# Performance work log

Measured on AMD Instinct MI355X. Metric: run time of the kernel, lower is better.

Reference implementation:

```python
import jax, jax.numpy as jnp
import numpy as np

KERNEL_MUL = 2.0
KERNEL_NUM = 5


def setup_inputs() -> dict:
    key = jax.random.key(0)
    k1, k2 = jax.random.split(key)
    N, D = 4096, 256
    source = jax.random.normal(k1, (N, D), dtype=jnp.float32)
    target = jax.random.normal(k2, (N, D), dtype=jnp.float32)
    return {"source": source, "target": target}


def _gaussian_kernel_sum(source, target):
    # total: [2N, D]
    total = jnp.concatenate([source, target], axis=0)
    n = total.shape[0]
    sq = jnp.sum(total * total, axis=1)  # [2N]
    L2 = sq[:, None] + sq[None, :] - 2.0 * (total @ total.T)  # [2N, 2N]
    # Bandwidth from detached mean of off-diagonal-normalized sum (torch uses .data)
    bandwidth = jax.lax.stop_gradient(jnp.sum(L2)) / (n * n - n)
    bandwidth = bandwidth / (KERNEL_MUL ** (KERNEL_NUM // 2))
    kernels = sum(
        jnp.exp(-L2 / (bandwidth * (KERNEL_MUL ** i))) for i in range(KERNEL_NUM)
    )
    return kernels


def reference(source, target):
    b = source.shape[0]
    K = _gaussian_kernel_sum(source, target)
    XX = jnp.mean(K[:b, :b])
    YY = jnp.mean(K[b:, b:])
    XY = jnp.mean(K[:b, b:])
    YX = jnp.mean(K[b:, :b])
    return XX + YY - XY - YX
```

## Files before the change

### kernel.cpp

```cpp
#include <hip/hip_runtime.h>


#define NROWS 8192
#define HALF  4096
#define DIM   256
#define CONVB 256
#define NTILE 1056

typedef __bf16 bf16x8 __attribute__((ext_vector_type(8)));
typedef float f32x4 __attribute__((ext_vector_type(4)));
typedef unsigned short ushort8 __attribute__((ext_vector_type(8)));

__device__ __forceinline__ const float* row_ptr(const float* src, const float* tgt, int r) {
    return (r < HALF) ? (src + (size_t)r * DIM) : (tgt + (size_t)(r - HALF) * DIM);
}

__device__ __forceinline__ unsigned short bf16_rne(float x) {
    unsigned int u = __builtin_bit_cast(unsigned int, x);
    return (unsigned short)((u + 0x7FFFu + ((u >> 16) & 1u)) >> 16);
}

__global__ __launch_bounds__(256) void k_conv(const float* __restrict__ src,
                                              const float* __restrict__ tgt,
                                              unsigned short* __restrict__ hi,
                                              float* __restrict__ sq,
                                              float* __restrict__ part,
                                              double* __restrict__ parts1,
                                              float* __restrict__ out) {
    __shared__ __align__(16) unsigned short sh_hi[32 * 32 * 8];
    __shared__ float4 cs[4][64];
    __shared__ double s1s[4];

    int w = threadIdx.x >> 6, lane = threadIdx.x & 63;
    int r0 = blockIdx.x * 32;
    int g  = lane >> 1, j = lane & 1;

    float4 v[8];
    #pragma unroll
    for (int i = 0; i < 8; ++i) {
        int row = r0 + w * 8 + i;
        v[i] = ((const float4*)row_ptr(src, tgt, row))[lane];
    }

    float4 csum = {0.f, 0.f, 0.f, 0.f};
    double s1w = 0.0;
    #pragma unroll
    for (int i = 0; i < 8; ++i) {
        int rl  = w * 8 + i;
        float xs[4] = {v[i].x, v[i].y, v[i].z, v[i].w};
        unsigned short hs[4];
        #pragma unroll
        for (int k = 0; k < 4; ++k) hs[k] = bf16_rne(xs[k]);
        ushort4 h4 = {hs[0], hs[1], hs[2], hs[3]};
        int so = (g * 32 + rl) * 8 + j * 4;
        *(ushort4*)&sh_hi[so] = h4;
        csum.x += xs[0]; csum.y += xs[1]; csum.z += xs[2]; csum.w += xs[3];
        float s = xs[0] * xs[0] + xs[1] * xs[1] + xs[2] * xs[2] + xs[3] * xs[3];
        #pragma unroll
        for (int off = 32; off; off >>= 1) s += __shfl_xor(s, off, 64);
        if (lane == 0) { sq[r0 + rl] = s; s1w += (double)s; }
    }
    __syncthreads();
    int panel = blockIdx.x >> 2, quarter = blockIdx.x & 3;
    #pragma unroll
    for (int c = threadIdx.x; c < 1024; c += 256) {
        int gg = c >> 5, r = c & 31;
        size_t goff = (((size_t)panel * 32 + gg) * 128 + quarter * 32 + r) * 8;
        *(ushort8*)&hi[goff] = *(const ushort8*)&sh_hi[c * 8];
    }
    cs[w][lane] = csum;
    if (lane == 0) s1s[w] = s1w;
    __syncthreads();
    if (w == 0) {
        float4 a = cs[0][lane], b = cs[1][lane], c = cs[2][lane], d = cs[3][lane];
        float4 tot = {a.x + b.x + c.x + d.x, a.y + b.y + c.y + d.y,
                      a.z + b.z + c.z + d.z, a.w + b.w + c.w + d.w};
        *(float4*)&part[(size_t)blockIdx.x * DIM + lane * 4] = tot;
        if (lane == 0) parts1[blockIdx.x] = s1s[0] + s1s[1] + s1s[2] + s1s[3];
    }
    if (blockIdx.x == 0 && threadIdx.x == 0) out[0] = 0.0f;
}

__global__ __launch_bounds__(256) void k_scale(const double* __restrict__ parts1,
                                               const float* __restrict__ part,
                                               float* __restrict__ scale) {
    __shared__ double sh[256];
    int t = threadIdx.x;
    sh[t] = parts1[t];
    __syncthreads();
    for (int off = 128; off; off >>= 1) {
        if (t < off) sh[t] += sh[t + off];
        __syncthreads();
    }
    double S1 = sh[0];
    __syncthreads();
    float c0 = 0.f, c1 = 0.f, c2 = 0.f, c3 = 0.f;
    #pragma unroll 16
    for (int b = 0; b < CONVB; b += 4) {
        c0 += part[(b + 0) * DIM + t];
        c1 += part[(b + 1) * DIM + t];
        c2 += part[(b + 2) * DIM + t];
        c3 += part[(b + 3) * DIM + t];
    }
    double c = (double)((c0 + c1) + (c2 + c3));
    sh[t] = c * c;
    __syncthreads();
    for (int off = 128; off; off >>= 1) {
        if (t < off) sh[t] += sh[t + off];
        __syncthreads();
    }
    if (t == 0) {
        double S2    = sh[0];
        double n     = (double)NROWS;
        double sumL2 = 2.0 * n * S1 - 2.0 * S2;
        double bw    = sumL2 / (n * n - n) / 4.0;
        *scale = (float)(-1.0 / (16.0 * bw * 0.69314718055994530942));
    }
}

__global__ __launch_bounds__(256, 2) void k_pairs(const unsigned short* __restrict__ hi,
                                                  const float* __restrict__ sq,
                                                  const float* __restrict__ scale_p,
                                                  float* __restrict__ out) {
    int id = blockIdx.x;
    int I = 0;
    for (;;) {
        int cnt = 64 - 2 * I;
        if (id < cnt) break;
        id -= cnt; ++I;
    }
    int J = 2 * I + id;

    __shared__ float wsum[4];

    int t    = threadIdx.x;
    int lane = t & 63;
    int w    = t >> 6;
    int lr   = lane & 15, lq = lane >> 4;
    int Pw   = 2 * I + (w >> 1);
    int hh   = w & 1;

    float wgt = (J == Pw) ? 1.0f : (J > Pw) ? 2.0f : 0.0f;
    float sgn = ((Pw < 32) == (J < 32)) ? 1.0f : -1.0f;

    size_t aBase = (size_t)Pw * 4096 + lq * 128 + hh * 64 + lr;
    size_t bBase = (size_t)J  * 4096 + lq * 128 + lr;
    const ushort8* pAh = (const ushort8*)hi + aBase;
    const ushort8* pBh = (const ushort8*)hi + bBase;

    f32x4 acc[4][8];
    #pragma unroll
    for (int m = 0; m < 4; ++m)
        #pragma unroll
        for (int n = 0; n < 8; ++n) acc[m][n] = (f32x4){0.f, 0.f, 0.f, 0.f};

    #pragma unroll
    for (int it = 0; it < DIM / 32; ++it) {
        bf16x8 aH[4], bH[8];
        #pragma unroll
        for (int m = 0; m < 4; ++m)
            aH[m] = __builtin_bit_cast(bf16x8, pAh[it * 512 + m * 16]);
        #pragma unroll
        for (int n = 0; n < 8; ++n)
            bH[n] = __builtin_bit_cast(bf16x8, pBh[it * 512 + n * 16]);
        #pragma unroll
        for (int m = 0; m < 4; ++m)
            #pragma unroll
            for (int n = 0; n < 8; ++n)
                acc[m][n] = __builtin_amdgcn_mfma_f32_16x16x32_bf16(aH[m], bH[n], acc[m][n], 0, 0, 0);
    }

    float scale = *scale_p;
    int ro_eff = Pw * 128 + hh * 64;
    int co_eff = J * 128;
    float4 sqa4[4];
    float  sqbv[8];
    #pragma unroll
    for (int m = 0; m < 4; ++m) sqa4[m] = *(const float4*)&sq[ro_eff + m * 16 + lq * 4];
    #pragma unroll
    for (int n = 0; n < 8; ++n) sqbv[n] = sq[co_eff + n * 16 + lr];

    float tsum = 0.0f;
    #pragma unroll
    for (int m = 0; m < 4; ++m) {
        float sa[4] = {sqa4[m].x, sqa4[m].y, sqa4[m].z, sqa4[m].w};
        #pragma unroll
        for (int n = 0; n < 8; ++n) {
            #pragma unroll
            for (int r = 0; r < 4; ++r) {
                float L2  = sa[r] + sqbv[n] - 2.0f * acc[m][n][r];
                float u   = __builtin_amdgcn_exp2f(scale * L2);
                float u2  = u * u;
                float u4  = u2 * u2;
                float u8  = u4 * u4;
                float u16 = u8 * u8;
                tsum += u + u2 + u4 + u8 + u16;
            }
        }
    }

    #pragma unroll
    for (int off = 32; off; off >>= 1) tsum += __shfl_xor(tsum, off, 64);
    if (lane == 0) wsum[w] = tsum * sgn * wgt;
    __syncthreads();
    if (t == 0) {
        float tot = wsum[0] + wsum[1] + wsum[2] + wsum[3];
        atomicAdd(out, tot * (1.0f / ((float)HALF * (float)HALF)));
    }
}

extern "C" void kernel_launch(void* const* d_in, const int* in_sizes, int n_in,
                              void* d_out, int out_size, void* d_ws, size_t ws_size,
                              hipStream_t stream) {
    const float* src = (const float*)d_in[0];
    const float* tgt = (const float*)d_in[1];
    float* out = (float*)d_out;

    char* ws = (char*)d_ws;
    float*  scale  = (float*)(ws + 16);
    float*  sq     = (float*)(ws + 64);
    float*  part   = (float*)(ws + 64 + 32768);
    double* parts1 = (double*)(ws + 64 + 32768 + 262144);
    unsigned short* hi = (unsigned short*)(ws + 297024);

    k_conv <<<CONVB, 256, 0, stream>>>(src, tgt, hi, sq, part, parts1, out);
    k_scale<<<1, 256, 0, stream>>>(parts1, part, scale);
    k_pairs<<<NTILE, 256, 0, stream>>>(hi, sq, scale, out);
}
```

Measured before the change: 108.1 us.

## Fuse conversion, bandwidth, and pair kernels into one cooperative persistent kernel

Replaces the three-kernel pipeline with one cooperative launch of 512 persistent blocks. Each block converts its rows to bf16, waits at a grid sync, and atomically adds column sums into 8 partial buffers. It then runs its MFMA tiles and spin-waits on a counter for the bandwidth scale only before the first exp, so the first matmul overlaps the reduction. This removes two kernel launches and the single-block scale kernel, at the cost of a grid barrier, atomics, a spin-wait, and uneven tile counts per block (1056 tiles over 512 blocks).

Result: slower. 181.8 us (+68.2%).

```diff
diff --git a/kernel.cpp b/kernel.cpp
--- a/kernel.cpp
+++ b/kernel.cpp
@@ -1,4 +1,5 @@
 #include <hip/hip_runtime.h>
+#include <hip/hip_cooperative_groups.h>
 
 
 #define NROWS 8192
@@ -6,6 +7,7 @@
 #define DIM   256
 #define CONVB 256
 #define NTILE 1056
+#define GRID  512
 
 typedef __bf16 bf16x8 __attribute__((ext_vector_type(8)));
 typedef float f32x4 __attribute__((ext_vector_type(4)));
@@ -18,6 +20,191 @@
 __device__ __forceinline__ unsigned short bf16_rne(float x) {
     unsigned int u = __builtin_bit_cast(unsigned int, x);
     return (unsigned short)((u + 0x7FFFu + ((u >> 16) & 1u)) >> 16);
+}
+
+__global__ __launch_bounds__(256, 2) void k_fused(
+        const float* __restrict__ src, const float* __restrict__ tgt,
+        unsigned short* __restrict__ hi, float* __restrict__ sq,
+        float* __restrict__ colsumP,
+        double* __restrict__ s1dP,
+        unsigned int* __restrict__ cnt,
+        float* __restrict__ out) {
+    __shared__ __align__(16) unsigned short sh_hi[16 * 32 * 8];
+    __shared__ float4 cs[4][64];
+    __shared__ double s1s[4];
+    __shared__ float wsum[4];
+
+    int t = threadIdx.x, w = t >> 6, lane = t & 63;
+
+    int r0 = blockIdx.x * 16;
+    int g = lane >> 1, jj = lane & 1;
+
+    float4 v[4];
+    #pragma unroll
+    for (int i = 0; i < 4; ++i)
+        v[i] = ((const float4*)row_ptr(src, tgt, r0 + w * 4 + i))[lane];
+
+    if (blockIdx.x == 0) {
+        #pragma unroll
+        for (int k = 0; k < 8; ++k) colsumP[k * DIM + t] = 0.0f;
+        if (t < 8) s1dP[t] = 0.0;
+        if (t == 0) { *cnt = 0u; out[0] = 0.0f; }
+    }
+
+    float4 csum = {0.f, 0.f, 0.f, 0.f};
+    double s1w = 0.0;
+    #pragma unroll
+    for (int i = 0; i < 4; ++i) {
+        int rl = w * 4 + i;
+        float xs[4] = {v[i].x, v[i].y, v[i].z, v[i].w};
+        unsigned short hs[4];
+        #pragma unroll
+        for (int k = 0; k < 4; ++k) hs[k] = bf16_rne(xs[k]);
+        ushort4 h4 = {hs[0], hs[1], hs[2], hs[3]};
+        *(ushort4*)&sh_hi[(g * 16 + rl) * 8 + jj * 4] = h4;
+        csum.x += xs[0]; csum.y += xs[1]; csum.z += xs[2]; csum.w += xs[3];
+        float s = xs[0]*xs[0] + xs[1]*xs[1] + xs[2]*xs[2] + xs[3]*xs[3];
+        #pragma unroll
+        for (int off = 32; off; off >>= 1) s += __shfl_xor(s, off, 64);
+        if (lane == 0) { sq[r0 + rl] = s; s1w += (double)s; }
+    }
+    __syncthreads();
+    {
+        int panel = r0 >> 7, rowbase = r0 & 127;
+        #pragma unroll
+        for (int c = t; c < 512; c += 256) {
+            int gg = c >> 4, r = c & 15;
+            size_t goff = (((size_t)panel * 32 + gg) * 128 + rowbase + r) * 8;
+            *(ushort8*)&hi[goff] = *(const ushort8*)&sh_hi[(gg * 16 + r) * 8];
+        }
+    }
+    cs[w][lane] = csum;
+    if (lane == 0) s1s[w] = s1w;
+    __syncthreads();
+    float4 tot = {0.f, 0.f, 0.f, 0.f};
+    double s1blk = 0.0;
+    if (w == 0) {
+        float4 a = cs[0][lane], b = cs[1][lane], c2 = cs[2][lane], d = cs[3][lane];
+        tot.x = a.x + b.x + c2.x + d.x; tot.y = a.y + b.y + c2.y + d.y;
+        tot.z = a.z + b.z + c2.z + d.z; tot.w = a.w + b.w + c2.w + d.w;
+        s1blk = s1s[0] + s1s[1] + s1s[2] + s1s[3];
+    }
+
+    cooperative_groups::this_grid().sync();
+
+    if (w == 0) {
+        float* cp = colsumP + (blockIdx.x & 7) * DIM + lane * 4;
+        float d0 = atomicAdd(cp + 0, tot.x);
+        float d1 = atomicAdd(cp + 1, tot.y);
+        float d2 = atomicAdd(cp + 2, tot.z);
+        float d3 = atomicAdd(cp + 3, tot.w);
+        float dep = (d0 + d1) + (d2 + d3);
+        if (lane == 0) dep += (float)atomicAdd(&s1dP[blockIdx.x & 7], s1blk);
+        asm volatile("" :: "v"(dep) : "memory");
+        if (lane == 0) atomicAdd(cnt, 1u);
+    }
+
+    int lr = lane & 15, lq = lane >> 4;
+    float scale_f = 0.0f, wtot = 0.0f;
+    bool have = false;
+
+    for (int tile = blockIdx.x; tile < NTILE; tile += GRID) {
+        int id = tile, I = 0;
+        for (;;) { int cnt2 = 64 - 2 * I; if (id < cnt2) break; id -= cnt2; ++I; }
+        int J  = 2 * I + id;
+        int Pw = 2 * I + (w >> 1);
+        int hh = w & 1;
+
+        float wgt = (J == Pw) ? 1.0f : (J > Pw) ? 2.0f : 0.0f;
+        float sgn = ((Pw < 32) == (J < 32)) ? 1.0f : -1.0f;
+
+        size_t aBase = (size_t)Pw * 4096 + lq * 128 + hh * 64 + lr;
+        size_t bBase = (size_t)J  * 4096 + lq * 128 + lr;
+        const ushort8* pAh = (const ushort8*)hi + aBase;
+        const ushort8* pBh = (const ushort8*)hi + bBase;
+
+        f32x4 acc[4][8];
+        #pragma unroll
+        for (int m = 0; m < 4; ++m)
+            #pragma unroll
+            for (int n = 0; n < 8; ++n) acc[m][n] = (f32x4){0.f, 0.f, 0.f, 0.f};
+
+        #pragma unroll
+        for (int it = 0; it < DIM / 32; ++it) {
+            bf16x8 aH[4], bH[8];
+            #pragma unroll
+            for (int m = 0; m < 4; ++m)
+                aH[m] = __builtin_bit_cast(bf16x8, pAh[it * 512 + m * 16]);
+            #pragma unroll
+            for (int n = 0; n < 8; ++n)
+                bH[n] = __builtin_bit_cast(bf16x8, pBh[it * 512 + n * 16]);
+            #pragma unroll
+            for (int m = 0; m < 4; ++m)
+                #pragma unroll
+                for (int n = 0; n < 8; ++n)
+                    acc[m][n] = __builtin_amdgcn_mfma_f32_16x16x32_bf16(aH[m], bH[n], acc[m][n], 0, 0, 0);
+        }
+
+        if (!have) {
+            while (atomicAdd(cnt, 0u) < (unsigned)GRID) __builtin_amdgcn_s_sleep(2);
+            float4 c4 = {0.f, 0.f, 0.f, 0.f};
+            #pragma unroll
+            for (int k = 0; k < 8; ++k) {
+                float4 vv = *(const float4*)&colsumP[k * DIM + lane * 4];
+                c4.x += vv.x; c4.y += vv.y; c4.z += vv.z; c4.w += vv.w;
+            }
+            double s2 = (double)c4.x * c4.x + (double)c4.y * c4.y
+                      + (double)c4.z * c4.z + (double)c4.w * c4.w;
+            #pragma unroll
+            for (int off = 32; off; off >>= 1) s2 += __shfl_xor(s2, off, 64);
+            double S1 = 0.0;
+            #pragma unroll
+            for (int k = 0; k < 8; ++k) S1 += s1dP[k];
+            double nd    = (double)NROWS;
+            double sumL2 = 2.0 * nd * S1 - 2.0 * s2;
+            double bw    = sumL2 / (nd * nd - nd) / 4.0;
+            scale_f = (float)(-1.0 / (16.0 * bw * 0.69314718055994530942));
+            have = true;
+        }
+
+        int ro_eff = Pw * 128 + hh * 64;
+        int co_eff = J * 128;
+        float4 sqa4[4];
+        float  sqbv[8];
+        #pragma unroll
+        for (int m = 0; m < 4; ++m) sqa4[m] = *(const float4*)&sq[ro_eff + m * 16 + lq * 4];
+        #pragma unroll
+        for (int n = 0; n < 8; ++n) sqbv[n] = sq[co_eff + n * 16 + lr];
+
+        float tsum = 0.0f;
+        #pragma unroll
+        for (int m = 0; m < 4; ++m) {
+            float sa[4] = {sqa4[m].x, sqa4[m].y, sqa4[m].z, sqa4[m].w};
+            #pragma unroll
+            for (int n = 0; n < 8; ++n) {
+                #pragma unroll
+                for (int r = 0; r < 4; ++r) {
+                    float L2  = sa[r] + sqbv[n] - 2.0f * acc[m][n][r];
+                    float u   = __builtin_amdgcn_exp2f(scale_f * L2);
+                    float u2  = u * u;
+                    float u4  = u2 * u2;
+                    float u8  = u4 * u4;
+                    float u16 = u8 * u8;
+                    tsum += u + u2 + u4 + u8 + u16;
+                }
+            }
+        }
+        #pragma unroll
+        for (int off = 32; off; off >>= 1) tsum += __shfl_xor(tsum, off, 64);
+        wtot += tsum * sgn * wgt;
+    }
+
+    if (lane == 0) wsum[w] = wtot;
+    __syncthreads();
+    if (t == 0) {
+        float tot4 = wsum[0] + wsum[1] + wsum[2] + wsum[3];
+        atomicAdd(out, tot4 * (1.0f / ((float)HALF * (float)HALF)));
+    }
 }
 
 __global__ __launch_bounds__(256) void k_conv(const float* __restrict__ src,
@@ -215,15 +402,30 @@
     const float* src = (const float*)d_in[0];
     const float* tgt = (const float*)d_in[1];
     float* out = (float*)d_out;
-
     char* ws = (char*)d_ws;
-    float*  scale  = (float*)(ws + 16);
-    float*  sq     = (float*)(ws + 64);
-    float*  part   = (float*)(ws + 64 + 32768);
-    double* parts1 = (double*)(ws + 64 + 32768 + 262144);
-    unsigned short* hi = (unsigned short*)(ws + 297024);
-
-    k_conv <<<CONVB, 256, 0, stream>>>(src, tgt, hi, sq, part, parts1, out);
-    k_scale<<<1, 256, 0, stream>>>(parts1, part, scale);
-    k_pairs<<<NTILE, 256, 0, stream>>>(hi, sq, scale, out);
-}
+
+    unsigned int* cnt   = (unsigned int*)(ws + 0);
+    double* s1dP        = (double*)(ws + 64);
+    float*  colsumP     = (float*)(ws + 128);
+    float*  sqF         = (float*)(ws + 8448);
+    unsigned short* hiF = (unsigned short*)(ws + 65536);
+
+    void* args[8];
+    args[0] = (void*)&src;  args[1] = (void*)&tgt;
+    args[2] = (void*)&hiF;  args[3] = (void*)&sqF;
+    args[4] = (void*)&colsumP; args[5] = (void*)&s1dP;
+    args[6] = (void*)&cnt;  args[7] = (void*)&out;
+
+    hipError_t e = hipLaunchCooperativeKernel((const void*)k_fused, dim3(GRID),
+                                              dim3(256), args, 0, stream);
+    if (e != hipSuccess) {
+        float*  scale  = (float*)(ws + 16);
+        float*  sq     = (float*)(ws + 64);
+        float*  part   = (float*)(ws + 64 + 32768);
+        double* parts1 = (double*)(ws + 64 + 32768 + 262144);
+        unsigned short* hi = (unsigned short*)(ws + 297024);
+        k_conv <<<CONVB, 256, 0, stream>>>(src, tgt, hi, sq, part, parts1, out);
+        k_scale<<<1, 256, 0, stream>>>(parts1, part, scale);
+        k_pairs<<<NTILE, 256, 0, stream>>>(hi, sq, scale, out);
+    }
+}
```

## Switch pair kernel to 128x128 triangular tiles with register double-buffered loads

Applied to the files above, without the earlier changes.

Reassigns each block to one 128x128 upper-triangular tile, with each wave computing a 64x64 sub-tile instead of 64x128, so no tiles are computed only to be weighted by zero. Operand fragments for the next K step are prefetched into a second register buffer while the current MFMAs run. Smaller accumulators lower register pressure, but each wave loses operand reuse and the grid doubles in block count.

After: 111.0 us. 1.03x slower.

```diff
diff --git a/kernel.cpp b/kernel.cpp
--- a/kernel.cpp
+++ b/kernel.cpp
@@ -5,7 +5,7 @@
 #define HALF  4096
 #define DIM   256
 #define CONVB 256
-#define NTILE 1056
+#define NTILE 2080
 
 typedef __bf16 bf16x8 __attribute__((ext_vector_type(8)));
 typedef float f32x4 __attribute__((ext_vector_type(4)));
@@ -125,11 +125,11 @@
     int id = blockIdx.x;
     int I = 0;
     for (;;) {
-        int cnt = 64 - 2 * I;
+        int cnt = 64 - I;
         if (id < cnt) break;
         id -= cnt; ++I;
     }
-    int J = 2 * I + id;
+    int J = I + id;
 
     __shared__ float wsum[4];
 
@@ -137,55 +137,62 @@
     int lane = t & 63;
     int w    = t >> 6;
     int lr   = lane & 15, lq = lane >> 4;
-    int Pw   = 2 * I + (w >> 1);
-    int hh   = w & 1;
-
-    float wgt = (J == Pw) ? 1.0f : (J > Pw) ? 2.0f : 0.0f;
-    float sgn = ((Pw < 32) == (J < 32)) ? 1.0f : -1.0f;
-
-    size_t aBase = (size_t)Pw * 4096 + lq * 128 + hh * 64 + lr;
-    size_t bBase = (size_t)J  * 4096 + lq * 128 + lr;
+    int wr   = w >> 1, wc = w & 1;
+
+    float wgt = (J == I) ? 1.0f : 2.0f;
+    float sgn = ((I < 32) == (J < 32)) ? 1.0f : -1.0f;
+
+    size_t aBase = (size_t)I * 4096 + (size_t)lq * 128 + wr * 64 + lr;
+    size_t bBase = (size_t)J * 4096 + (size_t)lq * 128 + wc * 64 + lr;
     const ushort8* pAh = (const ushort8*)hi + aBase;
     const ushort8* pBh = (const ushort8*)hi + bBase;
 
-    f32x4 acc[4][8];
+    f32x4 acc[4][4];
     #pragma unroll
     for (int m = 0; m < 4; ++m)
         #pragma unroll
-        for (int n = 0; n < 8; ++n) acc[m][n] = (f32x4){0.f, 0.f, 0.f, 0.f};
+        for (int n = 0; n < 4; ++n) acc[m][n] = (f32x4){0.f, 0.f, 0.f, 0.f};
+
+    bf16x8 aH[2][4], bH[2][4];
+    #pragma unroll
+    for (int m = 0; m < 4; ++m) aH[0][m] = __builtin_bit_cast(bf16x8, pAh[m * 16]);
+    #pragma unroll
+    for (int n = 0; n < 4; ++n) bH[0][n] = __builtin_bit_cast(bf16x8, pBh[n * 16]);
 
     #pragma unroll
     for (int it = 0; it < DIM / 32; ++it) {
-        bf16x8 aH[4], bH[8];
+        int cur = it & 1, nxt = cur ^ 1;
+        if (it < DIM / 32 - 1) {
+            #pragma unroll
+            for (int m = 0; m < 4; ++m)
+                aH[nxt][m] = __builtin_bit_cast(bf16x8, pAh[(it + 1) * 512 + m * 16]);
+            #pragma unroll
+            for (int n = 0; n < 4; ++n)
+                bH[nxt][n] = __builtin_bit_cast(bf16x8, pBh[(it + 1) * 512 + n * 16]);
+        }
         #pragma unroll
         for (int m = 0; m < 4; ++m)
-            aH[m] = __builtin_bit_cast(bf16x8, pAh[it * 512 + m * 16]);
-        #pragma unroll
-        for (int n = 0; n < 8; ++n)
-            bH[n] = __builtin_bit_cast(bf16x8, pBh[it * 512 + n * 16]);
-        #pragma unroll
-        for (int m = 0; m < 4; ++m)
-            #pragma unroll
-            for (int n = 0; n < 8; ++n)
-                acc[m][n] = __builtin_amdgcn_mfma_f32_16x16x32_bf16(aH[m], bH[n], acc[m][n], 0, 0, 0);
+            #pragma unroll
+            for (int n = 0; n < 4; ++n)
+                acc[m][n] = __builtin_amdgcn_mfma_f32_16x16x32_bf16(aH[cur][m], bH[cur][n], acc[m][n], 0, 0, 0);
     }
 
     float scale = *scale_p;
-    int ro_eff = Pw * 128 + hh * 64;
-    int co_eff = J * 128;
+    int ro_eff = I * 128 + wr * 64;
+    int co_eff = J * 128 + wc * 64;
     float4 sqa4[4];
-    float  sqbv[8];
+    float  sqbv[4];
     #pragma unroll
     for (int m = 0; m < 4; ++m) sqa4[m] = *(const float4*)&sq[ro_eff + m * 16 + lq * 4];
     #pragma unroll
-    for (int n = 0; n < 8; ++n) sqbv[n] = sq[co_eff + n * 16 + lr];
+    for (int n = 0; n < 4; ++n) sqbv[n] = sq[co_eff + n * 16 + lr];
 
     float tsum = 0.0f;
     #pragma unroll
     for (int m = 0; m < 4; ++m) {
         float sa[4] = {sqa4[m].x, sqa4[m].y, sqa4[m].z, sqa4[m].w};
         #pragma unroll
-        for (int n = 0; n < 8; ++n) {
+        for (int n = 0; n < 4; ++n) {
             #pragma unroll
             for (int r = 0; r < 4; ++r) {
                 float L2  = sa[r] + sqbv[n] - 2.0f * acc[m][n][r];
@@ -201,11 +208,11 @@
 
     #pragma unroll
     for (int off = 32; off; off >>= 1) tsum += __shfl_xor(tsum, off, 64);
-    if (lane == 0) wsum[w] = tsum * sgn * wgt;
+    if (lane == 0) wsum[w] = tsum;
     __syncthreads();
     if (t == 0) {
         float tot = wsum[0] + wsum[1] + wsum[2] + wsum[3];
-        atomicAdd(out, tot * (1.0f / ((float)HALF * (float)HALF)));
+        atomicAdd(out, tot * sgn * wgt * (1.0f / ((float)HALF * (float)HALF)));
     }
 }
 
```
